# Kernel tuning notes

Hardware: AMD Instinct MI355X
Metric: run time of the kernel (lower is better)

## Reference

```python
import jax, jax.numpy as jnp
import numpy as np

N = 20000      # nodes
E = 320000     # edges
D = 512        # width
L = 4          # layers
VOCAB = 256
MAX_POS = 256
EPS = 1e-5


def setup_inputs() -> dict:
    key = jax.random.key(0)
    ks = jax.random.split(key, 12)
    tokens = jax.random.randint(ks[0], (N,), 0, VOCAB)
    pos = jax.random.randint(ks[1], (N,), 0, MAX_POS)
    edge_index = jax.random.randint(ks[2], (2, E), 0, N)
    vocab_emb = jax.random.normal(ks[3], (VOCAB, D), jnp.float32) * 0.05
    pos_emb = jax.random.normal(ks[4], (MAX_POS, D), jnp.float32) * 0.05
    bn_gamma = jnp.ones((L, D), jnp.float32)
    bn_beta = jnp.zeros((L, D), jnp.float32)
    bn_mean = jax.random.normal(ks[5], (L, D), jnp.float32) * 0.1
    bn_var = jax.random.uniform(ks[6], (L, D), jnp.float32, 0.5, 1.5)
    W_rel = jax.random.normal(ks[7], (L, D, D), jnp.float32) * (1.0 / np.sqrt(D))
    b_rel = jnp.zeros((L, D), jnp.float32)
    W_root = jax.random.normal(ks[8], (L, D, D), jnp.float32) * (1.0 / np.sqrt(D))
    return {
        "tokens": tokens, "pos": pos, "edge_index": edge_index,
        "vocab_emb": vocab_emb, "pos_emb": pos_emb,
        "bn_gamma": bn_gamma, "bn_beta": bn_beta,
        "bn_mean": bn_mean, "bn_var": bn_var,
        "W_rel": W_rel, "b_rel": b_rel, "W_root": W_root,
    }


def reference(tokens, pos, edge_index, vocab_emb, pos_emb,
              bn_gamma, bn_beta, bn_mean, bn_var, W_rel, b_rel, W_root):
    src, dst = edge_index[0], edge_index[1]
    # in-degree for mean aggregation (clamped to 1 like PyG mean aggr)
    deg = jax.ops.segment_sum(jnp.ones((E,), jnp.float32), dst, num_segments=N)
    deg = jnp.maximum(deg, 1.0)[:, None]                     # [N,1]

    x = vocab_emb[tokens] + pos_emb[pos]                     # [N,D]
    for l in range(L):
        # BatchNorm1d, eval mode with running stats
        inv = bn_gamma[l] * jax.lax.rsqrt(bn_var[l] + EPS)
        x = (x - bn_mean[l]) * inv + bn_beta[l]
        # GraphConv: W_root x_i + W_rel * mean_{j->i} x_j + b
        agg = jax.ops.segment_sum(x[src], dst, num_segments=N) / deg
        x = agg @ W_rel[l].T + b_rel[l] + x @ W_root[l].T
        x = jax.nn.relu(x)
    return x
```

## Files before the change

kernel.cpp:

```cpp
#include <hip/hip_runtime.h>
#include <cstdint>

#define EPS 1e-5f

typedef __attribute__((ext_vector_type(8))) short bf16x8;
typedef __attribute__((ext_vector_type(4))) float f32x4;

__device__ __forceinline__ unsigned short f2bf(float x) {
    uint32_t u = __float_as_uint(x);
    u += 0x7fffu + ((u >> 16) & 1u);
    return (unsigned short)(u >> 16);
}
__device__ __forceinline__ uint32_t pack2(float lo, float hi) {
    return (uint32_t)f2bf(lo) | ((uint32_t)f2bf(hi) << 16);
}
__device__ __forceinline__ float bflo(uint32_t p) { return __uint_as_float(p << 16); }
__device__ __forceinline__ float bfhi(uint32_t p) { return __uint_as_float(p & 0xffff0000u); }

__device__ __forceinline__ void async_ld16(const void* g, const void* l) {
    __builtin_amdgcn_global_load_lds(
        (const __attribute__((address_space(1))) uint32_t*)(uintptr_t)g,
        (__attribute__((address_space(3))) uint32_t*)(uint32_t)(uintptr_t)l,
        16, 0, 0);
}

__global__ __launch_bounds__(256) void zero_kernel(int* __restrict__ p, int n) {
    int i = blockIdx.x * 256 + threadIdx.x;
    if (i < n) p[i] = 0;
}

__global__ __launch_bounds__(256) void count_kernel(const int* __restrict__ ei,
                                                    int* __restrict__ deg, int E) {
    int e = blockIdx.x * 256 + threadIdx.x;
    if (e < E) atomicAdd(&deg[ei[E + e]], 1);
}

__global__ __launch_bounds__(1024) void scan_kernel(const int* __restrict__ deg,
                                                    int* __restrict__ offsets,
                                                    int* __restrict__ cursor,
                                                    float* __restrict__ deginv, int N) {
    __shared__ int part[1024];
    const int t = threadIdx.x;
    const int CH = (N + 1023) >> 10;
    const int base = t * CH;
    int s = 0;
    for (int j = 0; j < CH; ++j) {
        int idx = base + j;
        if (idx < N) s += deg[idx];
    }
    part[t] = s;
    __syncthreads();
    for (int off = 1; off < 1024; off <<= 1) {
        int add = (t >= off) ? part[t - off] : 0;
        __syncthreads();
        part[t] += add;
        __syncthreads();
    }
    int run = (t == 0) ? 0 : part[t - 1];
    for (int j = 0; j < CH; ++j) {
        int idx = base + j;
        if (idx < N) {
            offsets[idx] = run;
            cursor[idx]  = run;
            int dgi = deg[idx];
            deginv[idx] = 1.0f / (float)(dgi > 0 ? dgi : 1);
            run += dgi;
        }
    }
    if (t == 1023) offsets[N] = run;
}

__global__ __launch_bounds__(256) void fill_kernel(const int* __restrict__ ei,
                                                   int* __restrict__ cursor,
                                                   int* __restrict__ csr, int E) {
    int e = blockIdx.x * 256 + threadIdx.x;
    if (e < E) {
        int dd = ei[E + e];
        int slot = atomicAdd(&cursor[dd], 1);
        csr[slot] = ei[e];
    }
}

__global__ __launch_bounds__(256) void embed_bn_kernel(const int* __restrict__ tok,
                                                       const int* __restrict__ pos,
                                                       const float* __restrict__ vemb,
                                                       const float* __restrict__ pemb,
                                                       const float* __restrict__ gamma,
                                                       const float* __restrict__ beta,
                                                       const float* __restrict__ mean,
                                                       const float* __restrict__ var,
                                                       uint32_t* __restrict__ Acat, int N) {
    const int idx = blockIdx.x * 256 + threadIdx.x;
    if (idx >= N * 128) return;
    const int row = idx >> 7;
    const int c = (idx & 127) * 4;
    const int tk = tok[row];
    const int ps = pos[row];
    const float4 a = *(const float4*)&vemb[(size_t)tk * 512 + c];
    const float4 b = *(const float4*)&pemb[(size_t)ps * 512 + c];
    const float4 g = *(const float4*)&gamma[c];
    const float4 be = *(const float4*)&beta[c];
    const float4 mn = *(const float4*)&mean[c];
    const float4 vr = *(const float4*)&var[c];
    const float y0 = (a.x + b.x - mn.x) * (g.x * rsqrtf(vr.x + EPS)) + be.x;
    const float y1 = (a.y + b.y - mn.y) * (g.y * rsqrtf(vr.y + EPS)) + be.y;
    const float y2 = (a.z + b.z - mn.z) * (g.z * rsqrtf(vr.z + EPS)) + be.z;
    const float y3 = (a.w + b.w - mn.w) * (g.w * rsqrtf(vr.w + EPS)) + be.w;
    uint2 o;
    o.x = pack2(y0, y1);
    o.y = pack2(y2, y3);
    *(uint2*)&Acat[(size_t)row * 512 + (c >> 1)] = o;
}

__global__ __launch_bounds__(256) void castW_kernel(const float* __restrict__ Wroot,
                                                    const float* __restrict__ Wrel,
                                                    uint32_t* __restrict__ Wcat) {
    const int p = blockIdx.x * 256 + threadIdx.x;
    const int o  = p >> 9;
    const int dp = p & 511;
    float2 v;
    if (dp < 256) v = *(const float2*)&Wroot[(size_t)o * 512 + dp * 2];
    else          v = *(const float2*)&Wrel[(size_t)o * 512 + (dp - 256) * 2];
    Wcat[(size_t)o * 512 + dp] = pack2(v.x, v.y);
}

__global__ __launch_bounds__(256) void aggregate_kernel(uint32_t* __restrict__ Acat,
                                                        const int* __restrict__ offsets,
                                                        const int* __restrict__ csr,
                                                        const float* __restrict__ deginv,
                                                        int N) {
    const int node = blockIdx.x * 4 + (threadIdx.x >> 6);
    if (node >= N) return;
    const int lane = threadIdx.x & 63;
    const int col = lane * 4;
    const int beg = offsets[node];
    const int end = offsets[node + 1];
    float s[8] = {0.f, 0.f, 0.f, 0.f, 0.f, 0.f, 0.f, 0.f};
    int e = beg;
    for (; e + 4 <= end; e += 4) {
        const int i0 = csr[e];
        const int i1 = csr[e + 1];
        const int i2 = csr[e + 2];
        const int i3 = csr[e + 3];
        const uint4 p0 = *(const uint4*)&Acat[(size_t)i0 * 512 + col];
        const uint4 p1 = *(const uint4*)&Acat[(size_t)i1 * 512 + col];
        const uint4 p2 = *(const uint4*)&Acat[(size_t)i2 * 512 + col];
        const uint4 p3 = *(const uint4*)&Acat[(size_t)i3 * 512 + col];
        s[0] += bflo(p0.x) + bflo(p1.x) + bflo(p2.x) + bflo(p3.x);
        s[1] += bfhi(p0.x) + bfhi(p1.x) + bfhi(p2.x) + bfhi(p3.x);
        s[2] += bflo(p0.y) + bflo(p1.y) + bflo(p2.y) + bflo(p3.y);
        s[3] += bfhi(p0.y) + bfhi(p1.y) + bfhi(p2.y) + bfhi(p3.y);
        s[4] += bflo(p0.z) + bflo(p1.z) + bflo(p2.z) + bflo(p3.z);
        s[5] += bfhi(p0.z) + bfhi(p1.z) + bfhi(p2.z) + bfhi(p3.z);
        s[6] += bflo(p0.w) + bflo(p1.w) + bflo(p2.w) + bflo(p3.w);
        s[7] += bfhi(p0.w) + bfhi(p1.w) + bfhi(p2.w) + bfhi(p3.w);
    }
    for (; e < end; ++e) {
        const int i0 = csr[e];
        const uint4 p0 = *(const uint4*)&Acat[(size_t)i0 * 512 + col];
        s[0] += bflo(p0.x); s[1] += bfhi(p0.x);
        s[2] += bflo(p0.y); s[3] += bfhi(p0.y);
        s[4] += bflo(p0.z); s[5] += bfhi(p0.z);
        s[6] += bflo(p0.w); s[7] += bfhi(p0.w);
    }
    const float inv = deginv[node];
    uint4 o;
    o.x = pack2(s[0] * inv, s[1] * inv);
    o.y = pack2(s[2] * inv, s[3] * inv);
    o.z = pack2(s[4] * inv, s[5] * inv);
    o.w = pack2(s[6] * inv, s[7] * inv);
    *(uint4*)&Acat[(size_t)node * 512 + 256 + col] = o;
}

__global__ __launch_bounds__(512, 2)
void gemm_pipe(const unsigned short* __restrict__ A,
               const unsigned short* __restrict__ B,
               const float* __restrict__ bias,
               const float* __restrict__ gamma,
               const float* __restrict__ beta,
               const float* __restrict__ mean,
               const float* __restrict__ var,
               int last,
               float* __restrict__ C,
               unsigned short* __restrict__ Abn,
               int M, int mt, int rpx) {
    extern __shared__ unsigned short lds[];

    const int bid = blockIdx.x;
    const int xcd = bid & 7;
    const int slt = bid >> 3;
    const int bm  = xcd * rpx + (slt >> 2);
    const int bn  = slt & 3;
    if (bm >= mt) return;

    const int t    = threadIdx.x;
    const int lane = t & 63;
    const int wid  = t >> 6;
    const int wr   = wid >> 1;
    const int wc   = wid & 1;
    const int lm   = lane & 15;
    const int q    = lane >> 4;

    const int tr = t >> 3;
    const int sg = (t & 7) ^ (tr & 7);
    int r0 = bm * 256 + tr;        if (r0 >= M) r0 = M - 1;
    int r1 = bm * 256 + 64  + tr;  if (r1 >= M) r1 = M - 1;
    int r2 = bm * 256 + 128 + tr;  if (r2 >= M) r2 = M - 1;
    int r3 = bm * 256 + 192 + tr;  if (r3 >= M) r3 = M - 1;
    const unsigned short* gA0 = A + (size_t)r0 * 1024 + sg * 8;
    const unsigned short* gA1 = A + (size_t)r1 * 1024 + sg * 8;
    const unsigned short* gA2 = A + (size_t)r2 * 1024 + sg * 8;
    const unsigned short* gA3 = A + (size_t)r3 * 1024 + sg * 8;
    const unsigned short* gB0 = B + (size_t)(bn * 128 + tr)      * 1024 + sg * 8;
    const unsigned short* gB1 = B + (size_t)(bn * 128 + 64 + tr) * 1024 + sg * 8;
    const int ldst = t * 8;

#define STAGE_H0(KT, LP) do {                                          \
        async_ld16(gA0 + (KT) * 64, (LP) + 0 * 4096 + ldst);           \
        async_ld16(gA1 + (KT) * 64, (LP) + 1 * 4096 + ldst);           \
        async_ld16(gA2 + (KT) * 64, (LP) + 2 * 4096 + ldst);           \
    } while (0)
#define STAGE_H1(KT, LP) do {                                          \
        async_ld16(gA3 + (KT) * 64, (LP) + 3 * 4096 + ldst);           \
        async_ld16(gB0 + (KT) * 64, (LP) + 16384 + 0 * 4096 + ldst);   \
        async_ld16(gB1 + (KT) * 64, (LP) + 16384 + 1 * 4096 + ldst);   \
    } while (0)

    const int aB = (wr * 64 + lm) * 64;
    const int bB = 16384 + (wc * 64 + lm) * 64;
    const int sw = lm & 7;
    const int k0 = ((0 + q) ^ sw) * 8;
    const int k1 = ((4 + q) ^ sw) * 8;

    const f32x4 zero = {0.f, 0.f, 0.f, 0.f};
    f32x4 acc[4][4];
#pragma unroll
    for (int i = 0; i < 4; ++i)
#pragma unroll
        for (int j = 0; j < 4; ++j) acc[i][j] = zero;

#define MFMA_PHASE(KOFF) do {                                                   \
        bf16x8 afr[4], bfr[4];                                                  \
        _Pragma("unroll") for (int mf = 0; mf < 4; ++mf)                        \
            afr[mf] = *(const bf16x8*)&Lb[aB + mf * 1024 + (KOFF)];             \
        _Pragma("unroll") for (int nf = 0; nf < 4; ++nf)                        \
            bfr[nf] = *(const bf16x8*)&Lb[bB + nf * 1024 + (KOFF)];             \
        __builtin_amdgcn_s_setprio(1);                                          \
        _Pragma("unroll") for (int mf = 0; mf < 4; ++mf)                        \
            _Pragma("unroll") for (int nf = 0; nf < 4; ++nf)                    \
                acc[mf][nf] = __builtin_amdgcn_mfma_f32_16x16x32_bf16(          \
                    afr[mf], bfr[nf], acc[mf][nf], 0, 0, 0);                    \
        __builtin_amdgcn_s_setprio(0);                                          \
    } while (0)

    {
        unsigned short* L0 = lds;
        STAGE_H0(0, L0); STAGE_H1(0, L0);
        unsigned short* L1 = lds + 24576;
        STAGE_H0(1, L1); STAGE_H1(1, L1);
    }

#pragma unroll
    for (int kt = 0; kt < 16; ++kt) {
        unsigned short* Lb = lds + (kt % 3) * 24576;
        unsigned short* Ln = lds + ((kt + 2) % 3) * 24576;
        if (kt < 15) asm volatile("s_waitcnt vmcnt(6)" ::: "memory");
        else         asm volatile("s_waitcnt vmcnt(0)" ::: "memory");
        __builtin_amdgcn_s_barrier();
        __builtin_amdgcn_sched_barrier(0);

        if (kt + 2 < 16) STAGE_H0(kt + 2, Ln);
        MFMA_PHASE(k0);
        if (kt + 2 < 16) STAGE_H1(kt + 2, Ln);
        MFMA_PHASE(k1);
    }

#pragma unroll
    for (int nf = 0; nf < 4; ++nf) {
        const int col = bn * 128 + wc * 64 + nf * 16 + lm;
        const float bsv = bias[col];
        float bn_inv = 0.f, bn_mb = 0.f, bn_bt = 0.f;
        if (!last) {
            bn_inv = gamma[col] * rsqrtf(var[col] + EPS);
            bn_mb  = mean[col];
            bn_bt  = beta[col];
        }
#pragma unroll
        for (int mf = 0; mf < 4; ++mf) {
            const int row0 = bm * 256 + wr * 64 + mf * 16 + q * 4;
#pragma unroll
            for (int i = 0; i < 4; ++i) {
                const int row = row0 + i;
                if (row < M) {
                    float v = acc[mf][nf][i] + bsv;
                    v = v > 0.f ? v : 0.f;
                    if (last) {
                        C[(size_t)row * 512 + col] = v;
                    } else {
                        const float y = (v - bn_mb) * bn_inv + bn_bt;
                        Abn[(size_t)row * 1024 + col] = f2bf(y);
                    }
                }
            }
        }
    }
#undef STAGE_H0
#undef STAGE_H1
#undef MFMA_PHASE
}

extern "C" void kernel_launch(void* const* d_in, const int* in_sizes, int n_in,
                              void* d_out, int out_size, void* d_ws, size_t ws_size,
                              hipStream_t stream) {
    const int*   tokens = (const int*)d_in[0];
    const int*   posi   = (const int*)d_in[1];
    const int*   ei     = (const int*)d_in[2];
    const float* vemb   = (const float*)d_in[3];
    const float* pemb   = (const float*)d_in[4];
    const float* gamma  = (const float*)d_in[5];
    const float* beta   = (const float*)d_in[6];
    const float* mean   = (const float*)d_in[7];
    const float* var    = (const float*)d_in[8];
    const float* Wrel   = (const float*)d_in[9];
    const float* brel   = (const float*)d_in[10];
    const float* Wroot  = (const float*)d_in[11];

    const int N = in_sizes[0];
    const int E = in_sizes[2] / 2;
    float* out = (float*)d_out;

    char* w = (char*)d_ws;
    int*      deg     = (int*)(w);
    int*      offsets = (int*)(w + 80000);
    int*      cursor  = (int*)(w + 160016);
    float*    deginv  = (float*)(w + 240032);
    int*      csr     = (int*)(w + 320048);
    uint32_t* Acat    = (uint32_t*)(w + 1600064);
    uint32_t* Wcat    = (uint32_t*)(w + 42560064);

    static bool s_attr = false;
    if (!s_attr) {
        (void)hipFuncSetAttribute(reinterpret_cast<const void*>(gemm_pipe),
                                  hipFuncAttributeMaxDynamicSharedMemorySize, 147456);
        s_attr = true;
    }

    zero_kernel<<<(N + 255) / 256, 256, 0, stream>>>(deg, N);
    count_kernel<<<(E + 255) / 256, 256, 0, stream>>>(ei, deg, E);
    scan_kernel<<<1, 1024, 0, stream>>>(deg, offsets, cursor, deginv, N);
    fill_kernel<<<(E + 255) / 256, 256, 0, stream>>>(ei, cursor, csr, E);

    embed_bn_kernel<<<(N * 128 + 255) / 256, 256, 0, stream>>>(
        tokens, posi, vemb, pemb, gamma, beta, mean, var, Acat, N);

    const int mt  = (N + 255) >> 8;
    const int rpx = (mt + 7) >> 3;
    const int gb  = 8 * rpx * 4;

    for (int l = 0; l < 4; ++l) {
        const int last = (l == 3);
        castW_kernel<<<1024, 256, 0, stream>>>(Wroot + (size_t)l * 262144,
                                               Wrel + (size_t)l * 262144, Wcat);
        aggregate_kernel<<<(N + 3) / 4, 256, 0, stream>>>(Acat, offsets, csr, deginv, N);
        gemm_pipe<<<gb, 512, 147456, stream>>>(
            (const unsigned short*)Acat, (const unsigned short*)Wcat, brel + l * 512,
            gamma + (l + 1) * 512, beta + (l + 1) * 512,
            mean + (l + 1) * 512, var + (l + 1) * 512,
            last, out, (unsigned short*)Acat, N, mt, rpx);
    }
}
```

Before: 597.1 us.

## Retile GEMM to 256x256 blocks with 4-stage K=32 pipeline

The fused GEMM moves from 256x128 output tiles to 256x256, so each block holds 8x4 MFMA accumulators per wave and the A matrix is read from global memory half as often. The K loop is split into 32-wide slices with a 4-buffer LDS ring, and each half-phase issues its async loads between the fragment reads and the MFMAs. The cost is higher register pressure from 128 accumulator floats per lane, half as many blocks, and a barrier for every 32-wide K slice.

New measurement: 575.1 us. 1.04x faster.

```diff
diff --git a/kernel.cpp b/kernel.cpp
--- a/kernel.cpp
+++ b/kernel.cpp
@@ -173,111 +173,126 @@
 }
 
 __global__ __launch_bounds__(512, 2)
-void gemm_pipe(const unsigned short* __restrict__ A,
-               const unsigned short* __restrict__ B,
-               const float* __restrict__ bias,
-               const float* __restrict__ gamma,
-               const float* __restrict__ beta,
-               const float* __restrict__ mean,
-               const float* __restrict__ var,
-               int last,
-               float* __restrict__ C,
-               unsigned short* __restrict__ Abn,
-               int M, int mt, int rpx) {
+void gemm_8ph(const unsigned short* __restrict__ A,
+              const unsigned short* __restrict__ B,
+              const float* __restrict__ bias,
+              const float* __restrict__ gamma,
+              const float* __restrict__ beta,
+              const float* __restrict__ mean,
+              const float* __restrict__ var,
+              int last,
+              float* __restrict__ C,
+              unsigned short* __restrict__ Abn,
+              int M, int mt, int rpx) {
     extern __shared__ unsigned short lds[];
 
     const int bid = blockIdx.x;
-    const int xcd = bid & 7;
-    const int slt = bid >> 3;
-    const int bm  = xcd * rpx + (slt >> 2);
-    const int bn  = slt & 3;
+    const int bm  = (bid & 7) * rpx + (bid >> 4);
+    const int bn  = (bid >> 3) & 1;
     if (bm >= mt) return;
 
     const int t    = threadIdx.x;
     const int lane = t & 63;
     const int wid  = t >> 6;
-    const int wr   = wid >> 1;
-    const int wc   = wid & 1;
+    const int wr   = wid >> 2;
+    const int wc   = wid & 3;
     const int lm   = lane & 15;
     const int q    = lane >> 4;
 
-    const int tr = t >> 3;
-    const int sg = (t & 7) ^ (tr & 7);
-    int r0 = bm * 256 + tr;        if (r0 >= M) r0 = M - 1;
-    int r1 = bm * 256 + 64  + tr;  if (r1 >= M) r1 = M - 1;
-    int r2 = bm * 256 + 128 + tr;  if (r2 >= M) r2 = M - 1;
-    int r3 = bm * 256 + 192 + tr;  if (r3 >= M) r3 = M - 1;
-    const unsigned short* gA0 = A + (size_t)r0 * 1024 + sg * 8;
-    const unsigned short* gA1 = A + (size_t)r1 * 1024 + sg * 8;
-    const unsigned short* gA2 = A + (size_t)r2 * 1024 + sg * 8;
-    const unsigned short* gA3 = A + (size_t)r3 * 1024 + sg * 8;
-    const unsigned short* gB0 = B + (size_t)(bn * 128 + tr)      * 1024 + sg * 8;
-    const unsigned short* gB1 = B + (size_t)(bn * 128 + 64 + tr) * 1024 + sg * 8;
+    const int trow = t >> 2;
+    const int sg   = (t & 3) ^ ((t >> 3) & 3);
+    int a0 = bm * 256 + trow;       if (a0 >= M) a0 = M - 1;
+    int a1 = bm * 256 + 128 + trow; if (a1 >= M) a1 = M - 1;
+    const unsigned short* gA0 = A + (size_t)a0 * 1024 + sg * 8;
+    const unsigned short* gA1 = A + (size_t)a1 * 1024 + sg * 8;
+    const unsigned short* gB0 = B + (size_t)(bn * 256 + trow) * 1024 + sg * 8;
+    const unsigned short* gB1 = B + (size_t)(bn * 256 + 128 + trow) * 1024 + sg * 8;
     const int ldst = t * 8;
 
-#define STAGE_H0(KT, LP) do {                                          \
-        async_ld16(gA0 + (KT) * 64, (LP) + 0 * 4096 + ldst);           \
-        async_ld16(gA1 + (KT) * 64, (LP) + 1 * 4096 + ldst);           \
-        async_ld16(gA2 + (KT) * 64, (LP) + 2 * 4096 + ldst);           \
+#define STAGE_A(J, BUF) do {                                                   \
+        async_ld16(gA0 + (J) * 32, lds + (BUF) * 16384 + ldst);                \
+        async_ld16(gA1 + (J) * 32, lds + (BUF) * 16384 + 4096 + ldst);         \
     } while (0)
-#define STAGE_H1(KT, LP) do {                                          \
-        async_ld16(gA3 + (KT) * 64, (LP) + 3 * 4096 + ldst);           \
-        async_ld16(gB0 + (KT) * 64, (LP) + 16384 + 0 * 4096 + ldst);   \
-        async_ld16(gB1 + (KT) * 64, (LP) + 16384 + 1 * 4096 + ldst);   \
+#define STAGE_B(J, BUF) do {                                                   \
+        async_ld16(gB0 + (J) * 32, lds + (BUF) * 16384 + 8192 + ldst);         \
+        async_ld16(gB1 + (J) * 32, lds + (BUF) * 16384 + 12288 + ldst);        \
     } while (0)
 
-    const int aB = (wr * 64 + lm) * 64;
-    const int bB = 16384 + (wc * 64 + lm) * 64;
-    const int sw = lm & 7;
-    const int k0 = ((0 + q) ^ sw) * 8;
-    const int k1 = ((4 + q) ^ sw) * 8;
+    const int asw  = (q ^ ((lm >> 1) & 3)) * 8;
+    const int aoff = (wr * 128 + lm) * 32 + asw;
+    const int boff = 8192 + (wc * 64 + lm) * 32 + asw;
 
     const f32x4 zero = {0.f, 0.f, 0.f, 0.f};
-    f32x4 acc[4][4];
-#pragma unroll
-    for (int i = 0; i < 4; ++i)
+    f32x4 acc[8][4];
+#pragma unroll
+    for (int i = 0; i < 8; ++i)
 #pragma unroll
         for (int j = 0; j < 4; ++j) acc[i][j] = zero;
 
-#define MFMA_PHASE(KOFF) do {                                                   \
-        bf16x8 afr[4], bfr[4];                                                  \
-        _Pragma("unroll") for (int mf = 0; mf < 4; ++mf)                        \
-            afr[mf] = *(const bf16x8*)&Lb[aB + mf * 1024 + (KOFF)];             \
-        _Pragma("unroll") for (int nf = 0; nf < 4; ++nf)                        \
-            bfr[nf] = *(const bf16x8*)&Lb[bB + nf * 1024 + (KOFF)];             \
+#define MFMA16(MH, AF, B0, B1, B2, B3)                                          \
         __builtin_amdgcn_s_setprio(1);                                          \
-        _Pragma("unroll") for (int mf = 0; mf < 4; ++mf)                        \
-            _Pragma("unroll") for (int nf = 0; nf < 4; ++nf)                    \
-                acc[mf][nf] = __builtin_amdgcn_mfma_f32_16x16x32_bf16(          \
-                    afr[mf], bfr[nf], acc[mf][nf], 0, 0, 0);                    \
-        __builtin_amdgcn_s_setprio(0);                                          \
+        _Pragma("unroll") for (int mf = 0; mf < 4; ++mf) {                      \
+            acc[(MH) * 4 + mf][0] = __builtin_amdgcn_mfma_f32_16x16x32_bf16(    \
+                AF[mf], B0, acc[(MH) * 4 + mf][0], 0, 0, 0);                    \
+            acc[(MH) * 4 + mf][1] = __builtin_amdgcn_mfma_f32_16x16x32_bf16(    \
+                AF[mf], B1, acc[(MH) * 4 + mf][1], 0, 0, 0);                    \
+            acc[(MH) * 4 + mf][2] = __builtin_amdgcn_mfma_f32_16x16x32_bf16(    \
+                AF[mf], B2, acc[(MH) * 4 + mf][2], 0, 0, 0);                    \
+            acc[(MH) * 4 + mf][3] = __builtin_amdgcn_mfma_f32_16x16x32_bf16(    \
+                AF[mf], B3, acc[(MH) * 4 + mf][3], 0, 0, 0);                    \
+        }                                                                       \
+        __builtin_amdgcn_s_setprio(0);
+
+#define HALF_BODY(JJ, JG, W0LIT, DOSTG) do {                                    \
+        const unsigned short* Lp = lds + (JJ) * 16384;                          \
+             \
+        asm volatile("s_waitcnt vmcnt(" W0LIT ")" ::: "memory");                \
+        __builtin_amdgcn_s_barrier();                                           \
+        __builtin_amdgcn_sched_barrier(0);                                      \
+        bf16x8 b0, b1, b2, b3;                                                  \
+        {                                                \
+            bf16x8 af[4];                                                       \
+            _Pragma("unroll") for (int mf = 0; mf < 4; ++mf)                    \
+                af[mf] = *(const bf16x8*)(Lp + aoff + mf * 512);                \
+            b0 = *(const bf16x8*)(Lp + boff + 0 * 512);                         \
+            b1 = *(const bf16x8*)(Lp + boff + 1 * 512);                         \
+            b2 = *(const bf16x8*)(Lp + boff + 2 * 512);                         \
+            b3 = *(const bf16x8*)(Lp + boff + 3 * 512);                         \
+            if (DOSTG) { STAGE_A((JG) + 3, ((JJ) + 3) & 3); }                   \
+            asm volatile("s_waitcnt lgkmcnt(0)" ::: "memory");                  \
+            __builtin_amdgcn_sched_barrier(0);                                  \
+            MFMA16(0, af, b0, b1, b2, b3)                                       \
+        }                                                                       \
+        {                                                \
+            bf16x8 af[4];                                                       \
+            _Pragma("unroll") for (int mf = 0; mf < 4; ++mf)                    \
+                af[mf] = *(const bf16x8*)(Lp + aoff + (4 + mf) * 512);          \
+            if (DOSTG) { STAGE_B((JG) + 3, ((JJ) + 3) & 3); }                   \
+            asm volatile("s_waitcnt lgkmcnt(0)" ::: "memory");                  \
+            __builtin_amdgcn_sched_barrier(0);                                  \
+            MFMA16(1, af, b0, b1, b2, b3)                                       \
+        }                                                                       \
     } while (0)
 
-    {
-        unsigned short* L0 = lds;
-        STAGE_H0(0, L0); STAGE_H1(0, L0);
-        unsigned short* L1 = lds + 24576;
-        STAGE_H0(1, L1); STAGE_H1(1, L1);
-    }
-
-#pragma unroll
-    for (int kt = 0; kt < 16; ++kt) {
-        unsigned short* Lb = lds + (kt % 3) * 24576;
-        unsigned short* Ln = lds + ((kt + 2) % 3) * 24576;
-        if (kt < 15) asm volatile("s_waitcnt vmcnt(6)" ::: "memory");
-        else         asm volatile("s_waitcnt vmcnt(0)" ::: "memory");
-        __builtin_amdgcn_s_barrier();
-        __builtin_amdgcn_sched_barrier(0);
-
-        if (kt + 2 < 16) STAGE_H0(kt + 2, Ln);
-        MFMA_PHASE(k0);
-        if (kt + 2 < 16) STAGE_H1(kt + 2, Ln);
-        MFMA_PHASE(k1);
-    }
+    STAGE_A(0, 0); STAGE_B(0, 0);
+    STAGE_A(1, 1); STAGE_B(1, 1);
+    STAGE_A(2, 2); STAGE_B(2, 2);
+
+    for (int jt = 0; jt < 7; ++jt) {
+        const int j0 = jt * 4;
+        HALF_BODY(0, j0 + 0, "8", 1);
+        HALF_BODY(1, j0 + 1, "8", 1);
+        HALF_BODY(2, j0 + 2, "8", 1);
+        HALF_BODY(3, j0 + 3, "8", 1);
+    }
+    HALF_BODY(0, 28, "8", 1);
+    HALF_BODY(1, 29, "8", 0);
+    HALF_BODY(2, 30, "4", 0);
+    HALF_BODY(3, 31, "0", 0);
 
 #pragma unroll
     for (int nf = 0; nf < 4; ++nf) {
-        const int col = bn * 128 + wc * 64 + nf * 16 + lm;
+        const int col = bn * 256 + wc * 64 + nf * 16 + lm;
         const float bsv = bias[col];
         float bn_inv = 0.f, bn_mb = 0.f, bn_bt = 0.f;
         if (!last) {
@@ -286,8 +301,8 @@
             bn_bt  = beta[col];
         }
 #pragma unroll
-        for (int mf = 0; mf < 4; ++mf) {
-            const int row0 = bm * 256 + wr * 64 + mf * 16 + q * 4;
+        for (int mf = 0; mf < 8; ++mf) {
+            const int row0 = bm * 256 + wr * 128 + mf * 16 + q * 4;
 #pragma unroll
             for (int i = 0; i < 4; ++i) {
                 const int row = row0 + i;
@@ -304,9 +319,10 @@
             }
         }
     }
-#undef STAGE_H0
-#undef STAGE_H1
-#undef MFMA_PHASE
+#undef STAGE_A
+#undef STAGE_B
+#undef MFMA16
+#undef HALF_BODY
 }
 
 extern "C" void kernel_launch(void* const* d_in, const int* in_sizes, int n_in,
@@ -340,8 +356,8 @@
 
     static bool s_attr = false;
     if (!s_attr) {
-        (void)hipFuncSetAttribute(reinterpret_cast<const void*>(gemm_pipe),
-                                  hipFuncAttributeMaxDynamicSharedMemorySize, 147456);
+        (void)hipFuncSetAttribute(reinterpret_cast<const void*>(gemm_8ph),
+                                  hipFuncAttributeMaxDynamicSharedMemorySize, 131072);
         s_attr = true;
     }
 
@@ -355,14 +371,14 @@
 
     const int mt  = (N + 255) >> 8;
     const int rpx = (mt + 7) >> 3;
-    const int gb  = 8 * rpx * 4;
+    const int gb  = 8 * rpx * 2;
 
     for (int l = 0; l < 4; ++l) {
         const int last = (l == 3);
         castW_kernel<<<1024, 256, 0, stream>>>(Wroot + (size_t)l * 262144,
                                                Wrel + (size_t)l * 262144, Wcat);
         aggregate_kernel<<<(N + 3) / 4, 256, 0, stream>>>(Acat, offsets, csr, deginv, N);
-        gemm_pipe<<<gb, 512, 147456, stream>>>(
+        gemm_8ph<<<gb, 512, 131072, stream>>>(
             (const unsigned short*)Acat, (const unsigned short*)Wcat, brel + l * 512,
             gamma + (l + 1) * 512, beta + (l + 1) * 512,
             mean + (l + 1) * 512, var + (l + 1) * 512,
```
